# Kernel optimization log

Measured on AMD Instinct MI355X. Metric: run time of the kernel, lower is better.

The kernel has to match this reference:

```python
import jax, jax.numpy as jnp
import numpy as np

HIDDEN = 1024
FFN = 2048
N_EXPERTS = 8
TOP_K = 2
BSZ, Q_LEN = 1, 2048


def setup_inputs() -> dict:
    key = jax.random.key(0)
    ks = jax.random.split(key, 8)
    T = BSZ * Q_LEN
    x = jax.random.normal(ks[0], (BSZ, Q_LEN, HIDDEN), dtype=jnp.float32)
    weights = jax.random.uniform(ks[1], (T, N_EXPERTS), dtype=jnp.float32)
    top_weights = jax.random.uniform(ks[2], (T, TOP_K), dtype=jnp.float32)
    top_experts = jax.random.randint(ks[3], (T, TOP_K), 0, N_EXPERTS, dtype=jnp.int64)
    s = 0.02
    w_up = jax.random.normal(ks[4], (N_EXPERTS, HIDDEN, FFN), dtype=jnp.float32) * s
    w_gate = jax.random.normal(ks[5], (N_EXPERTS, HIDDEN, FFN), dtype=jnp.float32) * s
    w_down = jax.random.normal(ks[6], (N_EXPERTS, FFN, HIDDEN), dtype=jnp.float32) * s
    return {"x": x, "weights": weights, "top_weights": top_weights,
            "top_experts": top_experts, "w_up": w_up, "w_gate": w_gate, "w_down": w_down}


def reference(x, weights, top_weights, top_experts, w_up, w_gate, w_down):
    # x: [B, S, H]; top_experts/top_weights: [T, K]; weights unused (parity with torch forward)
    B, S, H = x.shape
    E = w_up.shape[0]
    xf = x.reshape(-1, H)  # [T, H]
    # per-token combine weight for each expert: w_tok[t, e] = sum_k top_weights[t,k] * (top_experts[t,k]==e)
    onehot = jax.nn.one_hot(top_experts, E, dtype=x.dtype)  # [T, K, E]
    w_tok = jnp.einsum('tke,tk->te', onehot, top_weights)   # [T, E]

    def body(acc, ws):
        wu, wg, wd, we = ws  # [H,F], [H,F], [F,H], [T]
        h = jax.nn.silu(xf @ wu) * (xf @ wg)  # SwiGLU: act(up) * gate
        return acc + (h @ wd) * we[:, None], None

    out, _ = jax.lax.scan(body, jnp.zeros_like(xf), (w_up, w_gate, w_down, w_tok.T))
    return out.reshape(B, S, H)
```

## Files before the change

kernel.cpp:

```cpp
#include <hip/hip_runtime.h>
#include <hip/hip_bf16.h>
#include <stdint.h>

#define T_TOK 2048
#define HID   1024
#define FFN_  2048
#define NEXP  8
#define NPAIR 4096
#define MAXTILE 40
#define EXPELEM ((size_t)HID * FFN_)
#define NSLICE 16

typedef __bf16 bf16;
typedef __bf16 bf16x8 __attribute__((ext_vector_type(8)));
typedef __bf16 bf16x4 __attribute__((ext_vector_type(4)));
typedef float  f32x4  __attribute__((ext_vector_type(4)));
typedef float  f32x4v __attribute__((ext_vector_type(4)));
typedef unsigned int u32;

#define OFF_EXP   0
#define OFF_NT    64
#define OFF_TTE   128
#define OFF_TTM   512
#define OFF_TOK   1024
#define OFF_WGT   (OFF_TOK + 16384)
#define OFF_XG    65536
#define OFF_H1    (OFF_XG + (size_t)NPAIR*HID*2)
#define OFF_WT    (OFF_H1 + (size_t)NPAIR*FFN_*2)

__device__ __forceinline__ void gld16(const void* g, void* l) {
    __builtin_amdgcn_global_load_lds(
        (const __attribute__((address_space(1))) u32*)g,
        (__attribute__((address_space(3))) u32*)l, 16, 0, 0);
}

__global__ void __launch_bounds__(1024)
route_kernel(const uint32_t* __restrict__ te_raw,
             const float* __restrict__ top_w,
             int* __restrict__ expert_off,
             int* __restrict__ ntile_g,
             int* __restrict__ tte, int* __restrict__ ttm,
             int* __restrict__ tok, float* __restrict__ wgt)
{
    __shared__ int cnt[NSLICE][NEXP];
    __shared__ int off[NSLICE][NEXP];
    __shared__ int ebase[NEXP + 1];
    __shared__ int is64_s;
    int tid = threadIdx.x;
    int wv = tid >> 6, lane = tid & 63;

    if (wv == 0) {
        int bad = (te_raw[2 * lane + 1] != 0u);
        unsigned long long m = __ballot(bad);
        if (lane == 0) is64_s = (m == 0ull);
    }
    __syncthreads();
    int is64 = is64_s;

    int c[NEXP] = {0,0,0,0,0,0,0,0};
    int eids[4];
    #pragma unroll
    for (int it = 0; it < 4; ++it) {
        int p = wv * 256 + it * 64 + lane;
        int eid = is64 ? (int)te_raw[2*p] : (int)te_raw[p];
        eids[it] = eid;
        #pragma unroll
        for (int e = 0; e < NEXP; ++e) {
            unsigned long long m = __ballot(eid == e);
            c[e] += __popcll(m);
        }
    }
    if (lane == 0)
        #pragma unroll
        for (int e = 0; e < NEXP; ++e) cnt[wv][e] = c[e];
    __syncthreads();

    if (tid < NEXP) {
        int run = 0;
        for (int s = 0; s < NSLICE; ++s) { off[s][tid] = run; run += cnt[s][tid]; }
        ebase[tid] = run;
    }
    __syncthreads();
    if (tid == 0) {
        int s = 0;
        for (int e = 0; e < NEXP; ++e) { int t = ebase[e]; ebase[e] = s; expert_off[e] = s; s += t; }
        ebase[NEXP] = s; expert_off[NEXP] = s;
        int nt = 0;
        for (int e = 0; e < NEXP; ++e)
            for (int m = ebase[e]; m < ebase[e + 1]; m += 128) { tte[nt] = e; ttm[nt] = m; ++nt; }
        *ntile_g = nt;
    }
    __syncthreads();

    int roff[NEXP];
    #pragma unroll
    for (int e = 0; e < NEXP; ++e) roff[e] = ebase[e] + off[wv][e];
    #pragma unroll
    for (int it = 0; it < 4; ++it) {
        int p = wv * 256 + it * 64 + lane;
        int eid = eids[it];
        int dest = -1;
        #pragma unroll
        for (int e = 0; e < NEXP; ++e) {
            unsigned long long m = __ballot(eid == e);
            if (eid == e) dest = roff[e] + __popcll(m & ((1ull << lane) - 1ull));
            roff[e] += __popcll(m);
        }
        tok[dest] = p >> 1;
        wgt[dest] = top_w[p];
    }
}

__global__ void gather_kernel(const float* __restrict__ x,
                              const int* __restrict__ tok,
                              bf16* __restrict__ Xg)
{
    int p = blockIdx.x;
    int t = tok[p];
    const float4* src = (const float4*)(x + (size_t)t * HID);
    float4 v = src[threadIdx.x];
    bf16x4 o;
    o[0] = (bf16)v.x; o[1] = (bf16)v.y; o[2] = (bf16)v.z; o[3] = (bf16)v.w;
    *(bf16x4*)(Xg + (size_t)p * HID + threadIdx.x * 4) = o;
}

__global__ void __launch_bounds__(256)
transpose_v5(const float* __restrict__ in1, bf16* __restrict__ out1,
             const float* __restrict__ in2, bf16* __restrict__ out2,
             int nz1, int R, int C)
{
    __shared__ u32 tile32[4][64 * 32];
    int z = blockIdx.z;
    const float* in = (z < nz1) ? in1 : in2;
    bf16* o         = (z < nz1) ? out1 : out2;
    int e = (z < nz1) ? z : z - nz1;
    in += (size_t)e * R * C;
    o  += (size_t)e * R * C;
    int kt = blockIdx.x, nq = blockIdx.y;
    int k0 = kt * 64, c0 = nq * 256;
    int tid = threadIdx.x;
    int rbase = tid >> 6;
    int c4 = tid & 63;
    int grp = c4 >> 4, cq = c4 & 15;
    int fp0 = cq * 2;
    const float* base = in + (size_t)(k0 + rbase) * C + c0 + c4 * 4;
    f32x4v rb[16];
    #pragma unroll
    for (int it = 0; it < 16; ++it)
        rb[it] = __builtin_nontemporal_load((const f32x4v*)(base + (size_t)it * 4 * C));
    #pragma unroll
    for (int it = 0; it < 16; ++it) {
        int r = rbase + it * 4;
        union { bf16 h[2]; u32 w; } a, b;
        a.h[0] = (bf16)rb[it][0]; a.h[1] = (bf16)rb[it][1];
        b.h[0] = (bf16)rb[it][2]; b.h[1] = (bf16)rb[it][3];
        tile32[grp][r * 32 + (fp0       ^ (r & 31))] = a.w;
        tile32[grp][r * 32 + ((fp0 + 1) ^ (r & 31))] = b.w;
    }
    __syncthreads();
    int RT = R >> 6;
    #pragma unroll
    for (int it2 = 0; it2 < 8; ++it2) {
        int gg = it2 * 256 + tid;
        int group = gg >> 9, g = gg & 511;
        int f = g >> 3;
        int k8 = ((g & 7) ^ (f & 7)) * 8;
        union { bf16 h[8]; } pk;
        #pragma unroll
        for (int j = 0; j < 8; ++j) {
            u32 u = tile32[group][(k8 + j) * 32 + ((f >> 1) ^ ((k8 + j) & 31))];
            pk.h[j] = (f & 1) ? ((bf16*)&u)[1] : ((bf16*)&u)[0];
        }
        bf16* tbase = o + ((size_t)(nq * 4 + group) * RT + kt) * 4096;
        *(bf16x8*)(tbase + (size_t)g * 8) = *(bf16x8*)&pk;
    }
}

__global__ void __launch_bounds__(256)
moe_upgate(const bf16* __restrict__ Xg,
           const bf16* __restrict__ wuT, const bf16* __restrict__ wgT,
           const int* __restrict__ expert_off, const int* __restrict__ ntile_g,
           const int* __restrict__ tte, const int* __restrict__ ttm,
           bf16* __restrict__ H1)
{
    int ty = blockIdx.y;
    if (ty >= *ntile_g) return;
    int e = tte[ty];
    int m0 = ttm[ty];
    int p1 = expert_off[e + 1];
    int n0 = blockIdx.x * 64;
    __shared__ bf16 As [128 * 64];
    __shared__ bf16 Bus[64 * 64];
    __shared__ bf16 Bgs[64 * 64];
    int tid = threadIdx.x, lane = tid & 63, wv = tid >> 6;
    int wm = wv >> 1, wn = wv & 1;
    int l16 = lane & 15, lhi = lane >> 4;
    f32x4 accU[4][2] = {};
    f32x4 accG[4][2] = {};

    const bf16* aptr[4]; u32 alds[4];
    #pragma unroll
    for (int c = 0; c < 4; ++c) {
        int g = c * 256 + tid;
        int r = g >> 3, pos = g & 7;
        int gr = m0 + r; if (gr >= p1) gr = p1 - 1;
        int gsrc = pos ^ (r & 7);
        aptr[c] = Xg + (size_t)gr * HID + gsrc * 8;
        alds[c] = g * 16;
    }
    size_t tb0 = (size_t)e * EXPELEM + (size_t)(n0 >> 6) * (HID >> 6) * 4096;
    const bf16* buptr[2]; const bf16* bgptr[2]; u32 blds[2];
    #pragma unroll
    for (int c = 0; c < 2; ++c) {
        int g = c * 256 + tid;
        buptr[c] = wuT + tb0 + (size_t)g * 8;
        bgptr[c] = wgT + tb0 + (size_t)g * 8;
        blds[c] = g * 16;
    }
    u32 aro[2][4], bro[2][2];
    #pragma unroll
    for (int ks = 0; ks < 2; ++ks) {
        #pragma unroll
        for (int fm = 0; fm < 4; ++fm) {
            int r = wm * 64 + fm * 16 + l16;
            aro[ks][fm] = r * 128 + ((u32)((ks * 4 + lhi) ^ (r & 7))) * 16;
        }
        #pragma unroll
        for (int fn = 0; fn < 2; ++fn) {
            int fr = wn * 32 + fn * 16 + l16;
            bro[ks][fn] = fr * 128 + ((u32)((ks * 4 + lhi) ^ (fr & 7))) * 16;
        }
    }

    for (int t = 0; t < HID / 64; ++t) {
        #pragma unroll
        for (int c = 0; c < 4; ++c) { gld16(aptr[c], (char*)As + alds[c]); aptr[c] += 64; }
        #pragma unroll
        for (int c = 0; c < 2; ++c) {
            gld16(buptr[c], (char*)Bus + blds[c]); buptr[c] += 4096;
            gld16(bgptr[c], (char*)Bgs + blds[c]); bgptr[c] += 4096;
        }
        __syncthreads();
        #pragma unroll
        for (int ks = 0; ks < 2; ++ks) {
            bf16x8 af[4];
            #pragma unroll
            for (int fm = 0; fm < 4; ++fm)
                af[fm] = *(const bf16x8*)((char*)As + aro[ks][fm]);
            #pragma unroll
            for (int fn = 0; fn < 2; ++fn) {
                bf16x8 bu = *(const bf16x8*)((char*)Bus + bro[ks][fn]);
                bf16x8 bg = *(const bf16x8*)((char*)Bgs + bro[ks][fn]);
                #pragma unroll
                for (int fm = 0; fm < 4; ++fm) {
                    accU[fm][fn] = __builtin_amdgcn_mfma_f32_16x16x32_bf16(af[fm], bu, accU[fm][fn], 0, 0, 0);
                    accG[fm][fn] = __builtin_amdgcn_mfma_f32_16x16x32_bf16(af[fm], bg, accG[fm][fn], 0, 0, 0);
                }
            }
        }
        __syncthreads();
    }
    #pragma unroll
    for (int fm = 0; fm < 4; ++fm)
    #pragma unroll
    for (int fn = 0; fn < 2; ++fn)
    #pragma unroll
    for (int rg = 0; rg < 4; ++rg) {
        int r = m0 + wm * 64 + fm * 16 + lhi * 4 + rg;
        if (r < p1) {
            float u = accU[fm][fn][rg], g = accG[fm][fn][rg];
            float h = (u / (1.f + __expf(-u))) * g;
            int fc = n0 + wn * 32 + fn * 16 + l16;
            H1[(size_t)r * FFN_ + fc] = (bf16)h;
        }
    }
}

__global__ void __launch_bounds__(256)
moe_down(const bf16* __restrict__ H1, const bf16* __restrict__ wdT,
         const int* __restrict__ expert_off, const int* __restrict__ ntile_g,
         const int* __restrict__ tte, const int* __restrict__ ttm,
         const int* __restrict__ tok, const float* __restrict__ wgt,
         float* __restrict__ out)
{
    int ty = blockIdx.y;
    if (ty >= *ntile_g) return;
    int e = tte[ty];
    int m0 = ttm[ty];
    int p1 = expert_off[e + 1];
    int n0 = blockIdx.x * 64;
    __shared__ bf16 As[128 * 64];
    __shared__ bf16 Bs [64 * 64];
    __shared__ float wgt_s[128];
    __shared__ int   tok_s[128];
    int tid = threadIdx.x, lane = tid & 63, wv = tid >> 6;
    int wm = wv >> 1, wn = wv & 1;
    int l16 = lane & 15, lhi = lane >> 4;
    if (tid < 128) {
        int r = m0 + tid;
        if (r < p1) { wgt_s[tid] = wgt[r]; tok_s[tid] = tok[r]; }
        else        { wgt_s[tid] = 0.f;    tok_s[tid] = 0; }
    }
    f32x4 acc[4][2] = {};

    const bf16* aptr[4]; u32 alds[4];
    #pragma unroll
    for (int c = 0; c < 4; ++c) {
        int g = c * 256 + tid;
        int r = g >> 3, pos = g & 7;
        int gr = m0 + r; if (gr >= p1) gr = p1 - 1;
        int gsrc = pos ^ (r & 7);
        aptr[c] = H1 + (size_t)gr * FFN_ + gsrc * 8;
        alds[c] = g * 16;
    }
    size_t tb0 = (size_t)e * EXPELEM + (size_t)(n0 >> 6) * (FFN_ >> 6) * 4096;
    const bf16* bptr[2]; u32 blds[2];
    #pragma unroll
    for (int c = 0; c < 2; ++c) {
        int g = c * 256 + tid;
        bptr[c] = wdT + tb0 + (size_t)g * 8;
        blds[c] = g * 16;
    }
    u32 aro[2][4], bro[2][2];
    #pragma unroll
    for (int ks = 0; ks < 2; ++ks) {
        #pragma unroll
        for (int fm = 0; fm < 4; ++fm) {
            int r = wm * 64 + fm * 16 + l16;
            aro[ks][fm] = r * 128 + ((u32)((ks * 4 + lhi) ^ (r & 7))) * 16;
        }
        #pragma unroll
        for (int fn = 0; fn < 2; ++fn) {
            int fr = wn * 32 + fn * 16 + l16;
            bro[ks][fn] = fr * 128 + ((u32)((ks * 4 + lhi) ^ (fr & 7))) * 16;
        }
    }

    for (int t = 0; t < FFN_ / 64; ++t) {
        #pragma unroll
        for (int c = 0; c < 4; ++c) { gld16(aptr[c], (char*)As + alds[c]); aptr[c] += 64; }
        #pragma unroll
        for (int c = 0; c < 2; ++c) { gld16(bptr[c], (char*)Bs + blds[c]); bptr[c] += 4096; }
        __syncthreads();
        #pragma unroll
        for (int ks = 0; ks < 2; ++ks) {
            bf16x8 af[4];
            #pragma unroll
            for (int fm = 0; fm < 4; ++fm)
                af[fm] = *(const bf16x8*)((char*)As + aro[ks][fm]);
            #pragma unroll
            for (int fn = 0; fn < 2; ++fn) {
                bf16x8 bd = *(const bf16x8*)((char*)Bs + bro[ks][fn]);
                #pragma unroll
                for (int fm = 0; fm < 4; ++fm)
                    acc[fm][fn] = __builtin_amdgcn_mfma_f32_16x16x32_bf16(af[fm], bd, acc[fm][fn], 0, 0, 0);
            }
        }
        __syncthreads();
    }
    #pragma unroll
    for (int fm = 0; fm < 4; ++fm)
    #pragma unroll
    for (int fn = 0; fn < 2; ++fn)
    #pragma unroll
    for (int rg = 0; rg < 4; ++rg) {
        int rl = wm * 64 + fm * 16 + lhi * 4 + rg;
        if (m0 + rl < p1) {
            float v = acc[fm][fn][rg] * wgt_s[rl];
            atomicAdd(out + (size_t)tok_s[rl] * HID + n0 + wn * 32 + fn * 16 + l16, v);
        }
    }
}

extern "C" void kernel_launch(void* const* d_in, const int* in_sizes, int n_in,
                              void* d_out, int out_size, void* d_ws, size_t ws_size,
                              hipStream_t stream)
{
    const float*    x      = (const float*)d_in[0];
    const float*    top_w  = (const float*)d_in[2];
    const uint32_t* te     = (const uint32_t*)d_in[3];
    const float*    w_up   = (const float*)d_in[4];
    const float*    w_gate = (const float*)d_in[5];
    const float*    w_down = (const float*)d_in[6];
    float* out = (float*)d_out;
    char*  ws  = (char*)d_ws;

    int*   expert_off = (int*)(ws + OFF_EXP);
    int*   ntile_g    = (int*)(ws + OFF_NT);
    int*   tte        = (int*)(ws + OFF_TTE);
    int*   ttm        = (int*)(ws + OFF_TTM);
    int*   tok        = (int*)(ws + OFF_TOK);
    float* wgt        = (float*)(ws + OFF_WGT);
    bf16*  Xg         = (bf16*)(ws + OFF_XG);
    bf16*  H1         = (bf16*)(ws + OFF_H1);
    bf16*  WT         = (bf16*)(ws + OFF_WT);
    bf16*  wuT = WT;
    bf16*  wgT = WT + 8 * EXPELEM;
    bf16*  wdT = WT + 16 * EXPELEM;

    hipMemsetAsync(out, 0, (size_t)out_size * sizeof(float), stream);
    hipLaunchKernelGGL(route_kernel, dim3(1), dim3(1024), 0, stream,
                       te, top_w, expert_off, ntile_g, tte, ttm, tok, wgt);
    hipLaunchKernelGGL(gather_kernel, dim3(NPAIR), dim3(256), 0, stream,
                       x, tok, Xg);

    hipLaunchKernelGGL(transpose_v5, dim3(HID / 64, FFN_ / 256, 16), dim3(256), 0, stream,
                       w_up, wuT, w_gate, wgT, 8, HID, FFN_);
    hipLaunchKernelGGL(transpose_v5, dim3(FFN_ / 64, HID / 256, 8), dim3(256), 0, stream,
                       w_down, wdT, w_down, wdT, 8, FFN_, HID);

    hipLaunchKernelGGL(moe_upgate, dim3(FFN_ / 64, MAXTILE), dim3(256), 0, stream,
                       Xg, wuT, wgT, expert_off, ntile_g, tte, ttm, H1);
    hipLaunchKernelGGL(moe_down, dim3(HID / 64, MAXTILE), dim3(256), 0, stream,
                       H1, wdT, expert_off, ntile_g, tte, ttm, tok, wgt, out);
}
```

Before: 161.2 us.

## Fuse w_down transpose into up/gate GEMM launch as extra blocks

```diff
diff --git a/kernel.cpp b/kernel.cpp
--- a/kernel.cpp
+++ b/kernel.cpp
@@ -176,23 +176,76 @@
     }
 }
 
+#define NGEMM (MAXTILE * (FFN_ / 64))
 __global__ void __launch_bounds__(256)
-moe_upgate(const bf16* __restrict__ Xg,
-           const bf16* __restrict__ wuT, const bf16* __restrict__ wgT,
-           const int* __restrict__ expert_off, const int* __restrict__ ntile_g,
-           const int* __restrict__ tte, const int* __restrict__ ttm,
-           bf16* __restrict__ H1)
-{
-    int ty = blockIdx.y;
+fused_ug(const bf16* __restrict__ Xg,
+         const bf16* __restrict__ wuT, const bf16* __restrict__ wgT,
+         const int* __restrict__ expert_off, const int* __restrict__ ntile_g,
+         const int* __restrict__ tte, const int* __restrict__ ttm,
+         bf16* __restrict__ H1,
+         const float* __restrict__ Wd, bf16* __restrict__ wdT)
+{
+    __shared__ char ldsbuf[32768];
+    int bid = blockIdx.x;
+    int tid = threadIdx.x;
+
+    if (bid >= NGEMM) {
+        u32 (*tile32)[64 * 32] = (u32 (*)[64 * 32])ldsbuf;
+        int tb = bid - NGEMM;
+        int e = tb >> 7;
+        int rem = tb & 127;
+        int nq = rem >> 5, kt = rem & 31;
+        const float* in = Wd + (size_t)e * EXPELEM;
+        bf16* o = wdT + (size_t)e * EXPELEM;
+        int k0 = kt * 64, c0 = nq * 256;
+        int rbase = tid >> 6;
+        int c4 = tid & 63;
+        int grp = c4 >> 4, cq = c4 & 15;
+        int fp0 = cq * 2;
+        const float* base = in + (size_t)(k0 + rbase) * HID + c0 + c4 * 4;
+        f32x4v rb[16];
+        #pragma unroll
+        for (int it = 0; it < 16; ++it)
+            rb[it] = __builtin_nontemporal_load((const f32x4v*)(base + (size_t)it * 4 * HID));
+        #pragma unroll
+        for (int it = 0; it < 16; ++it) {
+            int r = rbase + it * 4;
+            union { bf16 h[2]; u32 w; } a, b;
+            a.h[0] = (bf16)rb[it][0]; a.h[1] = (bf16)rb[it][1];
+            b.h[0] = (bf16)rb[it][2]; b.h[1] = (bf16)rb[it][3];
+            tile32[grp][r * 32 + (fp0       ^ (r & 31))] = a.w;
+            tile32[grp][r * 32 + ((fp0 + 1) ^ (r & 31))] = b.w;
+        }
+        __syncthreads();
+        const int RT = FFN_ >> 6;
+        #pragma unroll
+        for (int it2 = 0; it2 < 8; ++it2) {
+            int gg = it2 * 256 + tid;
+            int group = gg >> 9, g = gg & 511;
+            int f = g >> 3;
+            int k8 = ((g & 7) ^ (f & 7)) * 8;
+            union { bf16 h[8]; } pk;
+            #pragma unroll
+            for (int j = 0; j < 8; ++j) {
+                u32 u = tile32[group][(k8 + j) * 32 + ((f >> 1) ^ ((k8 + j) & 31))];
+                pk.h[j] = (f & 1) ? ((bf16*)&u)[1] : ((bf16*)&u)[0];
+            }
+            bf16* tbase = o + ((size_t)(nq * 4 + group) * RT + kt) * 4096;
+            *(bf16x8*)(tbase + (size_t)g * 8) = *(bf16x8*)&pk;
+        }
+        return;
+    }
+
+    int ty = bid >> 5, bn = bid & 31;
     if (ty >= *ntile_g) return;
     int e = tte[ty];
     int m0 = ttm[ty];
     int p1 = expert_off[e + 1];
-    int n0 = blockIdx.x * 64;
-    __shared__ bf16 As [128 * 64];
-    __shared__ bf16 Bus[64 * 64];
-    __shared__ bf16 Bgs[64 * 64];
-    int tid = threadIdx.x, lane = tid & 63, wv = tid >> 6;
+    int n0 = bn * 64;
+    bf16* As  = (bf16*)ldsbuf;
+    bf16* Bus = (bf16*)(ldsbuf + 16384);
+    bf16* Bgs = (bf16*)(ldsbuf + 24576);
+    int lane = tid & 63, wv = tid >> 6;
     int wm = wv >> 1, wn = wv & 1;
     int l16 = lane & 15, lhi = lane >> 4;
     f32x4 accU[4][2] = {};
@@ -406,11 +459,11 @@
 
     hipLaunchKernelGGL(transpose_v5, dim3(HID / 64, FFN_ / 256, 16), dim3(256), 0, stream,
                        w_up, wuT, w_gate, wgT, 8, HID, FFN_);
-    hipLaunchKernelGGL(transpose_v5, dim3(FFN_ / 64, HID / 256, 8), dim3(256), 0, stream,
-                       w_down, wdT, w_down, wdT, 8, FFN_, HID);
-
-    hipLaunchKernelGGL(moe_upgate, dim3(FFN_ / 64, MAXTILE), dim3(256), 0, stream,
-                       Xg, wuT, wgT, expert_off, ntile_g, tte, ttm, H1);
+
+    hipLaunchKernelGGL(fused_ug, dim3(NGEMM + 1024), dim3(256), 0, stream,
+                       Xg, wuT, wgT, expert_off, ntile_g, tte, ttm, H1,
+                       w_down, wdT);
+
     hipLaunchKernelGGL(moe_down, dim3(HID / 64, MAXTILE), dim3(256), 0, stream,
                        H1, wdT, expert_off, ntile_g, tte, ttm, tok, wgt, out);
 }
```

Result: faster. 154.2 us (-4.3%).
